# Performance work log

Hardware: AMD Instinct MI355X
Metric: run time of the kernel (lower is better)

Reference implementation:

```python
import jax, jax.numpy as jnp
import numpy as np

NEG_SLOPE = 0.2
BN_EPS = 1e-5


def gat_conv(x, src, dst, num_nodes, W, att_src, att_dst, bias, concat):
    # x: [N, F_in]; W: [F_in, H*C]; att_src/att_dst: [H, C]
    H, C = att_src.shape
    h = (x @ W).reshape(num_nodes, H, C)                 # [N, H, C]
    a_src = jnp.einsum('nhc,hc->nh', h, att_src)          # [N, H]
    a_dst = jnp.einsum('nhc,hc->nh', h, att_dst)          # [N, H]
    e = a_src[src] + a_dst[dst]                           # [E, H]
    e = jax.nn.leaky_relu(e, NEG_SLOPE)
    # segment softmax over edges sharing the same destination node
    m = jax.ops.segment_max(e, dst, num_segments=num_nodes)   # [N, H]
    ex = jnp.exp(e - m[dst])
    denom = jax.ops.segment_sum(ex, dst, num_segments=num_nodes)  # [N, H]
    alpha = ex / (denom[dst] + 1e-16)                     # [E, H]
    msg = h[src] * alpha[:, :, None]                      # [E, H, C]
    out = jax.ops.segment_sum(msg, dst, num_segments=num_nodes)   # [N, H, C]
    if concat:
        return out.reshape(num_nodes, H * C) + bias
    return out.mean(axis=1) + bias


def batch_norm(x, gamma, beta):
    mu = x.mean(axis=0)
    var = x.var(axis=0)
    return (x - mu) * jax.lax.rsqrt(var + BN_EPS) * gamma + beta


def setup_inputs() -> dict:
    key = jax.random.key(0)
    ks = jax.random.split(key, 16)
    N, E, F_in, C, H, NC = 50000, 800000, 128, 16, 8, 2
    s = lambda k, shape, fan: jax.random.normal(k, shape, jnp.float32) * (1.0 / np.sqrt(fan))
    inp = {
        'x': jax.random.normal(ks[0], (N, F_in), jnp.float32),
        'edge_index': jax.random.randint(ks[1], (2, E), 0, N, jnp.int32),
        'W0': s(ks[2], (F_in, H * C), F_in),
        'att_src0': s(ks[3], (H, C), C),
        'att_dst0': s(ks[4], (H, C), C),
        'b0': jnp.zeros((H * C,), jnp.float32),
        'gamma0': jnp.ones((H * C,), jnp.float32),
        'beta0': jnp.zeros((H * C,), jnp.float32),
        'W1': s(ks[5], (H * C, H * C), H * C),
        'att_src1': s(ks[6], (H, C), C),
        'att_dst1': s(ks[7], (H, C), C),
        'b1': jnp.zeros((C,), jnp.float32),
        'gamma1': jnp.ones((C,), jnp.float32),
        'beta1': jnp.zeros((C,), jnp.float32),
        'Wc': s(ks[8], (C, NC), C),
        'bc': jnp.zeros((NC,), jnp.float32),
    }
    return inp


def reference(x, edge_index, W0, att_src0, att_dst0, b0, gamma0, beta0,
              W1, att_src1, att_dst1, b1, gamma1, beta1, Wc, bc):
    N = x.shape[0]
    loop = jnp.arange(N, dtype=edge_index.dtype)
    src = jnp.concatenate([edge_index[0], loop])  # add self-loops (PyG default)
    dst = jnp.concatenate([edge_index[1], loop])
    # layer 0: concat heads -> [N, H*C]
    h = gat_conv(x, src, dst, N, W0, att_src0, att_dst0, b0, concat=True)
    h = batch_norm(h, gamma0, beta0)
    h = jax.nn.elu(h)
    # layer 1: average heads -> [N, C]
    h = gat_conv(h, src, dst, N, W1, att_src1, att_dst1, b1, concat=False)
    h = batch_norm(h, gamma1, beta1)
    logits = h @ Wc + bc
    return logits
```

## Files before the change

kernel.cpp:

```cpp
#include <hip/hip_runtime.h>
#include <math.h>

#define NEG_SLOPE 0.2f
#define BN_EPS 1e-5f


__device__ __forceinline__ void edge_sd(const int* __restrict__ ei, int E, int eid, int& s, int& d) {
    if (eid < E) { s = ei[eid]; d = ei[E + eid]; }
    else         { s = d = eid - E; }
}

__device__ __forceinline__ float lrelu(float v) { return v > 0.f ? v : NEG_SLOPE * v; }

__device__ __forceinline__ unsigned short f2bf(float f) {
    unsigned u = __float_as_uint(f);
    u += 0x7fffu + ((u >> 16) & 1u);
    return (unsigned short)(u >> 16);
}

__global__ __launch_bounds__(256) void gemm128(const float* __restrict__ X,
                                               const float* __restrict__ W,
                                               unsigned short* __restrict__ Ybf,
                                               const float* __restrict__ att_s,
                                               const float* __restrict__ att_d,
                                               float* __restrict__ a_srcO,
                                               float* __restrict__ a_dstO,
                                               const float* __restrict__ bnmu,
                                               const float* __restrict__ bnrs,
                                               const float* __restrict__ gamma,
                                               const float* __restrict__ beta,
                                               int Nrows) {
    __shared__ float xs[64 * 128];
    int bm = blockIdx.x * 64;
    int tid = threadIdx.x;

    const float4* Xv = (const float4*)(X + (size_t)bm * 128);
    float4* xsv = (float4*)xs;
    if (bnmu == nullptr) {
        for (int i = tid; i < 64 * 32; i += 256) {
            int row = i >> 5;
            xsv[i] = (bm + row < Nrows) ? Xv[i] : make_float4(0.f, 0.f, 0.f, 0.f);
        }
    } else {
        for (int i = tid; i < 64 * 32; i += 256) {
            int row = i >> 5;
            int cb = (i & 31) * 4;
            float4 v = (bm + row < Nrows) ? Xv[i] : make_float4(0.f, 0.f, 0.f, 0.f);
            float4 m4 = *(const float4*)(bnmu + cb);
            float4 r4 = *(const float4*)(bnrs + cb);
            float4 g4 = *(const float4*)(gamma + cb);
            float4 b4 = *(const float4*)(beta + cb);
            v.x = (v.x - m4.x) * r4.x * g4.x + b4.x;
            v.y = (v.y - m4.y) * r4.y * g4.y + b4.y;
            v.z = (v.z - m4.z) * r4.z * g4.z + b4.z;
            v.w = (v.w - m4.w) * r4.w * g4.w + b4.w;
            v.x = v.x > 0.f ? v.x : expm1f(v.x);
            v.y = v.y > 0.f ? v.y : expm1f(v.y);
            v.z = v.z > 0.f ? v.z : expm1f(v.z);
            v.w = v.w > 0.f ? v.w : expm1f(v.w);
            xsv[i] = v;
        }
    }
    __syncthreads();

    int cq = tid & 31;
    int rg = tid >> 5;
    int lane = tid & 63;

    float acc[8][4];
#pragma unroll
    for (int r = 0; r < 8; r++)
#pragma unroll
        for (int j = 0; j < 4; j++) acc[r][j] = 0.f;

    const float* xbase = xs + (rg * 8) * 128;
#pragma unroll 2
    for (int k4 = 0; k4 < 32; k4++) {
        const float* wrow = W + k4 * 4 * 128 + cq * 4;
        float4 w0 = *(const float4*)(wrow);
        float4 w1 = *(const float4*)(wrow + 128);
        float4 w2 = *(const float4*)(wrow + 256);
        float4 w3 = *(const float4*)(wrow + 384);
#pragma unroll
        for (int r = 0; r < 8; r++) {
            float4 x4 = *(const float4*)(xbase + r * 128 + k4 * 4);
            acc[r][0] += x4.x * w0.x; acc[r][1] += x4.x * w0.y;
            acc[r][2] += x4.x * w0.z; acc[r][3] += x4.x * w0.w;
            acc[r][0] += x4.y * w1.x; acc[r][1] += x4.y * w1.y;
            acc[r][2] += x4.y * w1.z; acc[r][3] += x4.y * w1.w;
            acc[r][0] += x4.z * w2.x; acc[r][1] += x4.z * w2.y;
            acc[r][2] += x4.z * w2.z; acc[r][3] += x4.z * w2.w;
            acc[r][0] += x4.w * w3.x; acc[r][1] += x4.w * w3.y;
            acc[r][2] += x4.w * w3.z; acc[r][3] += x4.w * w3.w;
        }
    }

    int h = cq >> 2;
    float4 as4 = *(const float4*)(att_s + h * 16 + (cq & 3) * 4);
    float4 ad4 = *(const float4*)(att_d + h * 16 + (cq & 3) * 4);

#pragma unroll
    for (int r = 0; r < 8; r++) {
        int row = bm + rg * 8 + r;
        float ps = acc[r][0] * as4.x + acc[r][1] * as4.y + acc[r][2] * as4.z + acc[r][3] * as4.w;
        float pd = acc[r][0] * ad4.x + acc[r][1] * ad4.y + acc[r][2] * ad4.z + acc[r][3] * ad4.w;
        ps += __shfl_xor(ps, 1); ps += __shfl_xor(ps, 2);
        pd += __shfl_xor(pd, 1); pd += __shfl_xor(pd, 2);
        if (row < Nrows) {
            ushort4 pk;
            pk.x = f2bf(acc[r][0]);
            pk.y = f2bf(acc[r][1]);
            pk.z = f2bf(acc[r][2]);
            pk.w = f2bf(acc[r][3]);
            *(ushort4*)(Ybf + (size_t)row * 128 + cq * 4) = pk;
            if ((lane & 3) == 0) {
                a_srcO[row * 8 + h] = ps;
                a_dstO[row * 8 + h] = pd;
            }
        }
    }
}

__global__ void hist_kernel(const int* __restrict__ ei, int E, int Etot,
                            int* __restrict__ counts, int* __restrict__ rank) {
    int eid = blockIdx.x * 256 + threadIdx.x;
    if (eid >= Etot) return;
    int s, d;
    edge_sd(ei, E, eid, s, d);
    rank[eid] = atomicAdd(&counts[d], 1);
}

__global__ __launch_bounds__(256) void chunksum_kernel(const int* __restrict__ counts,
                                                       int* __restrict__ csum, int N) {
    __shared__ int red[256];
    int base = blockIdx.x * 1024;
    int s = 0;
    for (int i = threadIdx.x; i < 1024; i += 256) {
        int idx = base + i;
        s += (idx < N) ? counts[idx] : 0;
    }
    red[threadIdx.x] = s;
    __syncthreads();
#pragma unroll
    for (int st = 128; st > 0; st >>= 1) {
        if (threadIdx.x < st) red[threadIdx.x] += red[threadIdx.x + st];
        __syncthreads();
    }
    if (threadIdx.x == 0) csum[blockIdx.x] = red[0];
}

__global__ void chunkscan_kernel(int* __restrict__ csum, int nchunk) {
    int lane = threadIdx.x;
    int v = (lane < nchunk) ? csum[lane] : 0;
    int incl = v;
#pragma unroll
    for (int off = 1; off < 64; off <<= 1) {
        int t = __shfl_up(incl, off);
        if (lane >= off) incl += t;
    }
    if (lane < nchunk) csum[lane] = incl - v;
}

__global__ __launch_bounds__(1024) void scanfinal_kernel(const int* __restrict__ counts,
                                                         const int* __restrict__ csum,
                                                         int* __restrict__ rowptr, int N) {
    __shared__ int wsum[16], woff_s[16];
    int tid = threadIdx.x, lane = tid & 63, wid = tid >> 6;
    int idx = blockIdx.x * 1024 + tid;
    int v = (idx < N) ? counts[idx] : 0;
    int incl = v;
#pragma unroll
    for (int off = 1; off < 64; off <<= 1) {
        int t = __shfl_up(incl, off);
        if (lane >= off) incl += t;
    }
    if (lane == 63) wsum[wid] = incl;
    __syncthreads();
    if (wid == 0 && lane < 16) {
        int w = wsum[lane], iw = w;
#pragma unroll
        for (int off = 1; off < 16; off <<= 1) {
            int t = __shfl_up(iw, off);
            if (lane >= off) iw += t;
        }
        woff_s[lane] = iw - w;
    }
    __syncthreads();
    if (idx < N) rowptr[idx + 1] = csum[blockIdx.x] + woff_s[wid] + incl;
    if (blockIdx.x == 0 && tid == 0) rowptr[0] = 0;
}

__global__ void scatter_kernel(const int* __restrict__ ei, int E, int Etot,
                               const int* __restrict__ rowptr, const int* __restrict__ rank,
                               unsigned short* __restrict__ ssrc) {
    int eid = blockIdx.x * 256 + threadIdx.x;
    if (eid >= Etot) return;
    int s, d;
    edge_sd(ei, E, eid, s, d);
    ssrc[rowptr[d] + rank[eid]] = (unsigned short)s;
}

template <bool MEAN>
__global__ __launch_bounds__(256) void agg_kernel(const int* __restrict__ rowptr,
                                                  const unsigned short* __restrict__ ssrc,
                                                  const float* __restrict__ a_src,
                                                  const float* __restrict__ a_dst,
                                                  const unsigned short* __restrict__ Hbf,
                                                  float* __restrict__ outbuf, int N) {
    int wid = threadIdx.x >> 6;
    int dst = blockIdx.x * 4 + wid;
    if (dst >= N) return;
    int lane = threadIdx.x & 63;
    int j  = lane >> 3;
    int hj = lane & 7;
    int hf = lane >> 3;
    int f  = lane * 2;
    int start = rowptr[dst], end = rowptr[dst + 1];
    float adst = a_dst[dst * 8 + hj];

    float acc0 = 0.f, acc1 = 0.f, denl = 0.f;

    int i = start + j;
    int s = (i < end) ? (int)ssrc[i] : -1;
    float ar = (s >= 0) ? a_src[s * 8 + hj] : 0.f;

    for (int base = start; base < end; base += 8) {
        int sA[8];
#pragma unroll
        for (int j2 = 0; j2 < 8; j2++) sA[j2] = __shfl(s, j2 * 8);
        unsigned uA[8];
#pragma unroll
        for (int j2 = 0; j2 < 8; j2++)
            uA[j2] = (sA[j2] >= 0) ? *(const unsigned*)(Hbf + (size_t)sA[j2] * 128 + f) : 0u;

        int inext = base + 8 + j;
        int snext = (inext < end) ? (int)ssrc[inext] : -1;
        float anext = (snext >= 0) ? a_src[snext * 8 + hj] : 0.f;

        float w = (s >= 0) ? __expf(lrelu(ar + adst)) : 0.f;
        denl += w;
        float wA[8];
#pragma unroll
        for (int j2 = 0; j2 < 8; j2++) wA[j2] = __shfl(w, j2 * 8 + hf);

#pragma unroll
        for (int j2 = 0; j2 < 8; j2++) {
            acc0 += wA[j2] * __uint_as_float(uA[j2] << 16);
            acc1 += wA[j2] * __uint_as_float(uA[j2] & 0xffff0000u);
        }
        s = snext;
        ar = anext;
    }
#pragma unroll
    for (int off = 8; off < 64; off <<= 1) denl += __shfl_xor(denl, off);
    float den = __shfl(denl, hf);
    float inv = 1.f / (den + 1e-16f);
    if (!MEAN) {
        *(float2*)(outbuf + (size_t)dst * 128 + f) = make_float2(acc0 * inv, acc1 * inv);
    } else {
        float r0 = acc0 * inv, r1 = acc1 * inv;
#pragma unroll
        for (int off = 8; off < 64; off <<= 1) {
            r0 += __shfl_xor(r0, off);
            r1 += __shfl_xor(r1, off);
        }
        if (lane < 8)
            *(float2*)(outbuf + (size_t)dst * 16 + lane * 2) =
                make_float2(r0 * 0.125f, r1 * 0.125f);
    }
}

template <int C>
__global__ __launch_bounds__(256) void stats_part_kernel(const float* __restrict__ X, int Nrows,
                                                         float* __restrict__ partial,
                                                         int rows_per_block) {
    constexpr int GSZ = 256 / C;
    __shared__ float ls[256], lq[256];
    int c = threadIdx.x % C;
    int g = threadIdx.x / C;
    long base = (long)blockIdx.x * rows_per_block;
    long endr = base + rows_per_block;
    if (endr > Nrows) endr = Nrows;
    float s = 0.f, q = 0.f;
    for (long r = base + g; r < endr; r += GSZ) {
        float v = X[r * C + c];
        s += v;
        q += v * v;
    }
    ls[threadIdx.x] = s;
    lq[threadIdx.x] = q;
    __syncthreads();
#pragma unroll
    for (int st = GSZ / 2; st > 0; st >>= 1) {
        if (g < st) {
            ls[threadIdx.x] += ls[threadIdx.x + st * C];
            lq[threadIdx.x] += lq[threadIdx.x + st * C];
        }
        __syncthreads();
    }
    if (g == 0) {
        partial[(size_t)blockIdx.x * (2 * C) + c] = ls[c];
        partial[(size_t)blockIdx.x * (2 * C) + C + c] = lq[c];
    }
}

template <int C>
__global__ __launch_bounds__(1024) void stats_final_kernel(const float* __restrict__ partial,
                                                           int nblk, float invN,
                                                           float* __restrict__ mu,
                                                           float* __restrict__ rsig) {
    constexpr int G = 1024 / C;
    __shared__ float ls[1024], lq[1024];
    int c = threadIdx.x % C;
    int g = threadIdx.x / C;
    float s = 0.f, q = 0.f;
    for (int b = g; b < nblk; b += G) {
        s += partial[(size_t)b * (2 * C) + c];
        q += partial[(size_t)b * (2 * C) + C + c];
    }
    ls[threadIdx.x] = s;
    lq[threadIdx.x] = q;
    __syncthreads();
#pragma unroll
    for (int st = G / 2; st > 0; st >>= 1) {
        if (g < st) {
            ls[threadIdx.x] += ls[threadIdx.x + st * C];
            lq[threadIdx.x] += lq[threadIdx.x + st * C];
        }
        __syncthreads();
    }
    if (g == 0) {
        float m_ = ls[c] * invN;
        float v = lq[c] * invN - m_ * m_;
        mu[c] = m_;
        rsig[c] = rsqrtf(v + BN_EPS);
    }
}

__global__ void final_kernel(const float* __restrict__ out1,
                             const float* __restrict__ mu, const float* __restrict__ rsig,
                             const float* __restrict__ gamma, const float* __restrict__ beta,
                             const float* __restrict__ Wc, const float* __restrict__ bc,
                             float* __restrict__ out, int N) {
    int n = blockIdx.x * 256 + threadIdx.x;
    if (n >= N) return;
    float l0 = bc[0], l1 = bc[1];
#pragma unroll
    for (int c = 0; c < 16; c++) {
        float v = (out1[(size_t)n * 16 + c] - mu[c]) * rsig[c] * gamma[c] + beta[c];
        l0 += v * Wc[c * 2 + 0];
        l1 += v * Wc[c * 2 + 1];
    }
    out[(size_t)n * 2 + 0] = l0;
    out[(size_t)n * 2 + 1] = l1;
}

extern "C" void kernel_launch(void* const* d_in, const int* in_sizes, int n_in,
                              void* d_out, int out_size, void* d_ws, size_t ws_size,
                              hipStream_t stream) {
    const float* x   = (const float*)d_in[0];
    const int*   ei  = (const int*)d_in[1];
    const float* W0  = (const float*)d_in[2];
    const float* as0 = (const float*)d_in[3];
    const float* ad0 = (const float*)d_in[4];
    const float* g0  = (const float*)d_in[6];
    const float* be0 = (const float*)d_in[7];
    const float* W1  = (const float*)d_in[8];
    const float* as1 = (const float*)d_in[9];
    const float* ad1 = (const float*)d_in[10];
    const float* g1  = (const float*)d_in[12];
    const float* be1 = (const float*)d_in[13];
    const float* Wc  = (const float*)d_in[14];
    const float* bc  = (const float*)d_in[15];
    float* out = (float*)d_out;

    int N = in_sizes[0] / 128;
    int E = in_sizes[1] / 2;
    int Etot = E + N;

    char* ws = (char*)d_ws;
    size_t off = 0;
    auto walloc = [&](size_t bytes) -> void* {
        void* p = ws + off;
        off += (bytes + 255) & ~(size_t)255;
        return p;
    };
    float*          B       = (float*)walloc((size_t)N * 128 * 4);
    unsigned short* Hbf     = (unsigned short*)walloc((size_t)N * 128 * 2);
    float*          a_src   = (float*)walloc((size_t)N * 8 * 4);
    float*          a_dst   = (float*)walloc((size_t)N * 8 * 4);
    float*          out1    = (float*)walloc((size_t)N * 16 * 4);
    int*            counts  = (int*)walloc((size_t)N * 4);
    int*            rowptr  = (int*)walloc((size_t)(N + 1) * 4);
    int*            rank    = (int*)walloc((size_t)Etot * 4);
    int*            csum    = (int*)walloc(64 * 4);
    unsigned short* ssrc    = (unsigned short*)walloc((size_t)Etot * 2);
    float*          partial = (float*)walloc((size_t)256 * 256 * 4);
    float*          stats   = (float*)walloc(2 * 128 * 4);
    float* mu = stats, * rsig = stats + 128;

    dim3 b256(256);
    int gN64    = (N + 63) / 64;
    int gE      = (Etot + 255) / 256;
    int gAgg    = (N + 3) / 4;
    int nchunk  = (N + 1023) / 1024;
    const int SBLK = 256;
    int rpb = (N + SBLK - 1) / SBLK;

    hipMemsetAsync(counts, 0, (size_t)N * 4, stream);
    hist_kernel<<<gE, b256, 0, stream>>>(ei, E, Etot, counts, rank);
    chunksum_kernel<<<nchunk, b256, 0, stream>>>(counts, csum, N);
    chunkscan_kernel<<<1, 64, 0, stream>>>(csum, nchunk);
    scanfinal_kernel<<<nchunk, 1024, 0, stream>>>(counts, csum, rowptr, N);
    scatter_kernel<<<gE, b256, 0, stream>>>(ei, E, Etot, rowptr, rank, ssrc);

    gemm128<<<gN64, b256, 0, stream>>>(x, W0, Hbf, as0, ad0, a_src, a_dst,
                                       nullptr, nullptr, nullptr, nullptr, N);
    agg_kernel<false><<<gAgg, b256, 0, stream>>>(rowptr, ssrc, a_src, a_dst, Hbf, B, N);
    stats_part_kernel<128><<<SBLK, b256, 0, stream>>>(B, N, partial, rpb);
    stats_final_kernel<128><<<1, 1024, 0, stream>>>(partial, SBLK, 1.0f / N, mu, rsig);

    gemm128<<<gN64, b256, 0, stream>>>(B, W1, Hbf, as1, ad1, a_src, a_dst,
                                       mu, rsig, g0, be0, N);
    agg_kernel<true><<<gAgg, b256, 0, stream>>>(rowptr, ssrc, a_src, a_dst, Hbf, out1, N);
    stats_part_kernel<16><<<SBLK, b256, 0, stream>>>(out1, N, partial, rpb);
    stats_final_kernel<16><<<1, 1024, 0, stream>>>(partial, SBLK, 1.0f / N, mu, rsig);
    final_kernel<<<(N + 255) / 256, b256, 0, stream>>>(out1, mu, rsig, g1, be1, Wc, bc, out, N);
}
```

Baseline: 346.8 us.

## Restructure node GEMM with column-split grid, transposed weights, swizzled LDS tile

The 128-wide GEMM is split across 4 column groups via blockIdx.y. Each thread now computes one row by 8 columns, reading pre-transposed weights (a new small transpose kernel runs each call) as wave-uniform float4 loads. X tiles in LDS use an XOR swizzle to avoid bank conflicts on per-row reads. Attention dot products are reduced through LDS and the bf16 outputs are staged for coalesced 16-byte stores. The catch is that each block reloads and re-normalizes the full 64x128 X tile 4 times, and a kernel launch is added.

After: 496.0 us. +43.0%, slower.

```diff
diff --git a/kernel.cpp b/kernel.cpp
--- a/kernel.cpp
+++ b/kernel.cpp
@@ -18,8 +18,22 @@
     return (unsigned short)(u >> 16);
 }
 
+__global__ __launch_bounds__(256) void transpose_kernel(const float* __restrict__ W0,
+                                                        const float* __restrict__ W1,
+                                                        float* __restrict__ T0,
+                                                        float* __restrict__ T1) {
+    int b = blockIdx.x;
+    const float* S = (b & 4) ? W1 : W0;
+    float*       T = (b & 4) ? T1 : T0;
+    int part = b & 3;
+    for (int i = threadIdx.x; i < 4096; i += 256) {
+        int idx = part * 4096 + i;
+        T[(idx & 127) * 128 + (idx >> 7)] = S[idx];
+    }
+}
+
 __global__ __launch_bounds__(256) void gemm128(const float* __restrict__ X,
-                                               const float* __restrict__ W,
+                                               const float* __restrict__ Wt,
                                                unsigned short* __restrict__ Ybf,
                                                const float* __restrict__ att_s,
                                                const float* __restrict__ att_d,
@@ -32,19 +46,21 @@
                                                int Nrows) {
     __shared__ float xs[64 * 128];
     int bm = blockIdx.x * 64;
+    int cg = blockIdx.y;
     int tid = threadIdx.x;
 
     const float4* Xv = (const float4*)(X + (size_t)bm * 128);
     float4* xsv = (float4*)xs;
     if (bnmu == nullptr) {
-        for (int i = tid; i < 64 * 32; i += 256) {
-            int row = i >> 5;
-            xsv[i] = (bm + row < Nrows) ? Xv[i] : make_float4(0.f, 0.f, 0.f, 0.f);
+        for (int i = tid; i < 2048; i += 256) {
+            int row = i >> 5, c = i & 31;
+            float4 v = (bm + row < Nrows) ? Xv[i] : make_float4(0.f, 0.f, 0.f, 0.f);
+            xsv[((row << 5) | c) ^ (row & 7)] = v;
         }
     } else {
-        for (int i = tid; i < 64 * 32; i += 256) {
-            int row = i >> 5;
-            int cb = (i & 31) * 4;
+        for (int i = tid; i < 2048; i += 256) {
+            int row = i >> 5, c = i & 31;
+            int cb = c * 4;
             float4 v = (bm + row < Nrows) ? Xv[i] : make_float4(0.f, 0.f, 0.f, 0.f);
             float4 m4 = *(const float4*)(bnmu + cb);
             float4 r4 = *(const float4*)(bnrs + cb);
@@ -58,65 +74,74 @@
             v.y = v.y > 0.f ? v.y : expm1f(v.y);
             v.z = v.z > 0.f ? v.z : expm1f(v.z);
             v.w = v.w > 0.f ? v.w : expm1f(v.w);
-            xsv[i] = v;
-        }
-    }
-    __syncthreads();
-
-    int cq = tid & 31;
-    int rg = tid >> 5;
+            xsv[((row << 5) | c) ^ (row & 7)] = v;
+        }
+    }
+    __syncthreads();
+
+    int w = tid >> 6;
     int lane = tid & 63;
-
-    float acc[8][4];
-#pragma unroll
-    for (int r = 0; r < 8; r++)
-#pragma unroll
-        for (int j = 0; j < 4; j++) acc[r][j] = 0.f;
-
-    const float* xbase = xs + (rg * 8) * 128;
+    int c0 = cg * 32 + w * 8;
+
+    float acc[8];
+#pragma unroll
+    for (int j = 0; j < 8; j++) acc[j] = 0.f;
+
+    const float4* xr = (const float4*)xs;
+    const float* wbase = Wt + (size_t)c0 * 128;
+
 #pragma unroll 2
     for (int k4 = 0; k4 < 32; k4++) {
-        const float* wrow = W + k4 * 4 * 128 + cq * 4;
-        float4 w0 = *(const float4*)(wrow);
-        float4 w1 = *(const float4*)(wrow + 128);
-        float4 w2 = *(const float4*)(wrow + 256);
-        float4 w3 = *(const float4*)(wrow + 384);
-#pragma unroll
-        for (int r = 0; r < 8; r++) {
-            float4 x4 = *(const float4*)(xbase + r * 128 + k4 * 4);
-            acc[r][0] += x4.x * w0.x; acc[r][1] += x4.x * w0.y;
-            acc[r][2] += x4.x * w0.z; acc[r][3] += x4.x * w0.w;
-            acc[r][0] += x4.y * w1.x; acc[r][1] += x4.y * w1.y;
-            acc[r][2] += x4.y * w1.z; acc[r][3] += x4.y * w1.w;
-            acc[r][0] += x4.z * w2.x; acc[r][1] += x4.z * w2.y;
-            acc[r][2] += x4.z * w2.z; acc[r][3] += x4.z * w2.w;
-            acc[r][0] += x4.w * w3.x; acc[r][1] += x4.w * w3.y;
-            acc[r][2] += x4.w * w3.z; acc[r][3] += x4.w * w3.w;
-        }
-    }
-
-    int h = cq >> 2;
-    float4 as4 = *(const float4*)(att_s + h * 16 + (cq & 3) * 4);
-    float4 ad4 = *(const float4*)(att_d + h * 16 + (cq & 3) * 4);
-
-#pragma unroll
-    for (int r = 0; r < 8; r++) {
-        int row = bm + rg * 8 + r;
-        float ps = acc[r][0] * as4.x + acc[r][1] * as4.y + acc[r][2] * as4.z + acc[r][3] * as4.w;
-        float pd = acc[r][0] * ad4.x + acc[r][1] * ad4.y + acc[r][2] * ad4.z + acc[r][3] * ad4.w;
-        ps += __shfl_xor(ps, 1); ps += __shfl_xor(ps, 2);
-        pd += __shfl_xor(pd, 1); pd += __shfl_xor(pd, 2);
-        if (row < Nrows) {
-            ushort4 pk;
-            pk.x = f2bf(acc[r][0]);
-            pk.y = f2bf(acc[r][1]);
-            pk.z = f2bf(acc[r][2]);
-            pk.w = f2bf(acc[r][3]);
-            *(ushort4*)(Ybf + (size_t)row * 128 + cq * 4) = pk;
-            if ((lane & 3) == 0) {
-                a_srcO[row * 8 + h] = ps;
-                a_dstO[row * 8 + h] = pd;
-            }
+        float4 x4 = xr[((lane << 5) | k4) ^ (lane & 7)];
+#pragma unroll
+        for (int j = 0; j < 8; j++) {
+            float4 wj = *(const float4*)(wbase + j * 128 + k4 * 4);
+            acc[j] += x4.x * wj.x;
+            acc[j] += x4.y * wj.y;
+            acc[j] += x4.z * wj.z;
+            acc[j] += x4.w * wj.w;
+        }
+    }
+
+    __syncthreads();
+    float* sred = xs;
+    unsigned short* outls = (unsigned short*)(xs + 512);
+
+    int h = cg * 2 + (w >> 1);
+    int ao = (w & 1) * 8;
+    float4 asl = *(const float4*)(att_s + h * 16 + ao);
+    float4 ash = *(const float4*)(att_s + h * 16 + ao + 4);
+    float4 adl = *(const float4*)(att_d + h * 16 + ao);
+    float4 adh = *(const float4*)(att_d + h * 16 + ao + 4);
+    float ps = acc[0] * asl.x + acc[1] * asl.y + acc[2] * asl.z + acc[3] * asl.w
+             + acc[4] * ash.x + acc[5] * ash.y + acc[6] * ash.z + acc[7] * ash.w;
+    float pd = acc[0] * adl.x + acc[1] * adl.y + acc[2] * adl.z + acc[3] * adl.w
+             + acc[4] * adh.x + acc[5] * adh.y + acc[6] * adh.z + acc[7] * adh.w;
+    sred[(w * 64 + lane) * 2]     = ps;
+    sred[(w * 64 + lane) * 2 + 1] = pd;
+
+    ushort4 p0, p1;
+    p0.x = f2bf(acc[0]); p0.y = f2bf(acc[1]); p0.z = f2bf(acc[2]); p0.w = f2bf(acc[3]);
+    p1.x = f2bf(acc[4]); p1.y = f2bf(acc[5]); p1.z = f2bf(acc[6]); p1.w = f2bf(acc[7]);
+    *(ushort4*)(outls + lane * 32 + w * 8)     = p0;
+    *(ushort4*)(outls + lane * 32 + w * 8 + 4) = p1;
+    __syncthreads();
+
+    if (tid < 128) {
+        int r = tid & 63, p = tid >> 6;
+        if (bm + r < Nrows) {
+            float s0 = sred[((2 * p) * 64 + r) * 2]     + sred[((2 * p + 1) * 64 + r) * 2];
+            float d0 = sred[((2 * p) * 64 + r) * 2 + 1] + sred[((2 * p + 1) * 64 + r) * 2 + 1];
+            int hh = cg * 2 + p;
+            a_srcO[(size_t)(bm + r) * 8 + hh] = s0;
+            a_dstO[(size_t)(bm + r) * 8 + hh] = d0;
+        }
+    }
+    {
+        int r = tid >> 2, ch = tid & 3;
+        if (bm + r < Nrows) {
+            uint4 v = *(uint4*)(outls + r * 32 + ch * 8);
+            *(uint4*)(Ybf + (size_t)(bm + r) * 128 + cg * 32 + ch * 8) = v;
         }
     }
 }
@@ -397,15 +422,20 @@
     unsigned short* ssrc    = (unsigned short*)walloc((size_t)Etot * 2);
     float*          partial = (float*)walloc((size_t)256 * 256 * 4);
     float*          stats   = (float*)walloc(2 * 128 * 4);
+    float*          Wt0     = (float*)walloc((size_t)128 * 128 * 4);
+    float*          Wt1     = (float*)walloc((size_t)128 * 128 * 4);
     float* mu = stats, * rsig = stats + 128;
 
     dim3 b256(256);
     int gN64    = (N + 63) / 64;
+    dim3 gGemm(gN64, 4);
     int gE      = (Etot + 255) / 256;
     int gAgg    = (N + 3) / 4;
     int nchunk  = (N + 1023) / 1024;
     const int SBLK = 256;
     int rpb = (N + SBLK - 1) / SBLK;
+
+    transpose_kernel<<<8, b256, 0, stream>>>(W0, W1, Wt0, Wt1);
 
     hipMemsetAsync(counts, 0, (size_t)N * 4, stream);
     hist_kernel<<<gE, b256, 0, stream>>>(ei, E, Etot, counts, rank);
@@ -414,14 +444,14 @@
     scanfinal_kernel<<<nchunk, 1024, 0, stream>>>(counts, csum, rowptr, N);
     scatter_kernel<<<gE, b256, 0, stream>>>(ei, E, Etot, rowptr, rank, ssrc);
 
-    gemm128<<<gN64, b256, 0, stream>>>(x, W0, Hbf, as0, ad0, a_src, a_dst,
-                                       nullptr, nullptr, nullptr, nullptr, N);
+    gemm128<<<gGemm, b256, 0, stream>>>(x, Wt0, Hbf, as0, ad0, a_src, a_dst,
+                                        nullptr, nullptr, nullptr, nullptr, N);
     agg_kernel<false><<<gAgg, b256, 0, stream>>>(rowptr, ssrc, a_src, a_dst, Hbf, B, N);
     stats_part_kernel<128><<<SBLK, b256, 0, stream>>>(B, N, partial, rpb);
     stats_final_kernel<128><<<1, 1024, 0, stream>>>(partial, SBLK, 1.0f / N, mu, rsig);
 
-    gemm128<<<gN64, b256, 0, stream>>>(B, W1, Hbf, as1, ad1, a_src, a_dst,
-                                       mu, rsig, g0, be0, N);
+    gemm128<<<gGemm, b256, 0, stream>>>(B, Wt1, Hbf, as1, ad1, a_src, a_dst,
+                                        mu, rsig, g0, be0, N);
     agg_kernel<true><<<gAgg, b256, 0, stream>>>(rowptr, ssrc, a_src, a_dst, Hbf, out1, N);
     stats_part_kernel<16><<<SBLK, b256, 0, stream>>>(out1, N, partial, rpb);
     stats_final_kernel<16><<<1, 1024, 0, stream>>>(partial, SBLK, 1.0f / N, mu, rsig);
```

## Use split-bf16 MFMA (3-term) for the dense GEMMs instead of FP32 FMA

Applied to the files above, without the earlier changes.

The two 128x128 node-feature GEMMs now run on matrix cores with bf16 MFMA instructions. Activations and weights are split into high and low bf16 parts, and three MFMAs per tile keep accuracy close to fp32. A small pre-kernel splits and transposes W0 and W1 into hi/lo bf16 buffers. Results are staged in LDS to compute the attention projections and the bf16 output. The aim is to remove the FP32 FMA-bound GEMM cost, at the price of extra conversion work and a slight loss of precision.

Result: slower. 369.1 us (+6.4%).

```diff
diff --git a/kernel.cpp b/kernel.cpp
--- a/kernel.cpp
+++ b/kernel.cpp
@@ -3,6 +3,9 @@
 
 #define NEG_SLOPE 0.2f
 #define BN_EPS 1e-5f
+
+typedef __attribute__((ext_vector_type(8))) short short8v;
+typedef __attribute__((ext_vector_type(4))) float f32x4;
 
 
 __device__ __forceinline__ void edge_sd(const int* __restrict__ ei, int E, int eid, int& s, int& d) {
@@ -17,9 +20,35 @@
     u += 0x7fffu + ((u >> 16) & 1u);
     return (unsigned short)(u >> 16);
 }
+__device__ __forceinline__ float bfval(unsigned short u) {
+    return __uint_as_float(((unsigned)u) << 16);
+}
+
+__global__ __launch_bounds__(256) void wsplit_kernel(const float* __restrict__ W0,
+                                                     const float* __restrict__ W1,
+                                                     unsigned short* __restrict__ H0,
+                                                     unsigned short* __restrict__ L0,
+                                                     unsigned short* __restrict__ H1,
+                                                     unsigned short* __restrict__ L1) {
+    int b = blockIdx.x;
+    const float* S = (b & 4) ? W1 : W0;
+    unsigned short* H = (b & 4) ? H1 : H0;
+    unsigned short* L = (b & 4) ? L1 : L0;
+    int part = b & 3;
+    for (int i = threadIdx.x; i < 4096; i += 256) {
+        int idx = part * 4096 + i;
+        int k = idx >> 7, c = idx & 127;
+        float v = S[idx];
+        unsigned short h = f2bf(v);
+        unsigned short l = f2bf(v - bfval(h));
+        H[c * 128 + k] = h;
+        L[c * 128 + k] = l;
+    }
+}
 
 __global__ __launch_bounds__(256) void gemm128(const float* __restrict__ X,
-                                               const float* __restrict__ W,
+                                               const unsigned short* __restrict__ Wthi,
+                                               const unsigned short* __restrict__ Wtlo,
                                                unsigned short* __restrict__ Ybf,
                                                const float* __restrict__ att_s,
                                                const float* __restrict__ att_d,
@@ -30,92 +59,108 @@
                                                const float* __restrict__ gamma,
                                                const float* __restrict__ beta,
                                                int Nrows) {
-    __shared__ float xs[64 * 128];
+    __shared__ float hs[64 * 128];
     int bm = blockIdx.x * 64;
     int tid = threadIdx.x;
-
-    const float4* Xv = (const float4*)(X + (size_t)bm * 128);
-    float4* xsv = (float4*)xs;
-    if (bnmu == nullptr) {
-        for (int i = tid; i < 64 * 32; i += 256) {
-            int row = i >> 5;
-            xsv[i] = (bm + row < Nrows) ? Xv[i] : make_float4(0.f, 0.f, 0.f, 0.f);
-        }
-    } else {
-        for (int i = tid; i < 64 * 32; i += 256) {
-            int row = i >> 5;
-            int cb = (i & 31) * 4;
-            float4 v = (bm + row < Nrows) ? Xv[i] : make_float4(0.f, 0.f, 0.f, 0.f);
-            float4 m4 = *(const float4*)(bnmu + cb);
-            float4 r4 = *(const float4*)(bnrs + cb);
-            float4 g4 = *(const float4*)(gamma + cb);
-            float4 b4 = *(const float4*)(beta + cb);
-            v.x = (v.x - m4.x) * r4.x * g4.x + b4.x;
-            v.y = (v.y - m4.y) * r4.y * g4.y + b4.y;
-            v.z = (v.z - m4.z) * r4.z * g4.z + b4.z;
-            v.w = (v.w - m4.w) * r4.w * g4.w + b4.w;
-            v.x = v.x > 0.f ? v.x : expm1f(v.x);
-            v.y = v.y > 0.f ? v.y : expm1f(v.y);
-            v.z = v.z > 0.f ? v.z : expm1f(v.z);
-            v.w = v.w > 0.f ? v.w : expm1f(v.w);
-            xsv[i] = v;
-        }
-    }
-    __syncthreads();
-
-    int cq = tid & 31;
-    int rg = tid >> 5;
-    int lane = tid & 63;
-
-    float acc[8][4];
-#pragma unroll
-    for (int r = 0; r < 8; r++)
-#pragma unroll
-        for (int j = 0; j < 4; j++) acc[r][j] = 0.f;
-
-    const float* xbase = xs + (rg * 8) * 128;
-#pragma unroll 2
-    for (int k4 = 0; k4 < 32; k4++) {
-        const float* wrow = W + k4 * 4 * 128 + cq * 4;
-        float4 w0 = *(const float4*)(wrow);
-        float4 w1 = *(const float4*)(wrow + 128);
-        float4 w2 = *(const float4*)(wrow + 256);
-        float4 w3 = *(const float4*)(wrow + 384);
-#pragma unroll
-        for (int r = 0; r < 8; r++) {
-            float4 x4 = *(const float4*)(xbase + r * 128 + k4 * 4);
-            acc[r][0] += x4.x * w0.x; acc[r][1] += x4.x * w0.y;
-            acc[r][2] += x4.x * w0.z; acc[r][3] += x4.x * w0.w;
-            acc[r][0] += x4.y * w1.x; acc[r][1] += x4.y * w1.y;
-            acc[r][2] += x4.y * w1.z; acc[r][3] += x4.y * w1.w;
-            acc[r][0] += x4.z * w2.x; acc[r][1] += x4.z * w2.y;
-            acc[r][2] += x4.z * w2.z; acc[r][3] += x4.z * w2.w;
-            acc[r][0] += x4.w * w3.x; acc[r][1] += x4.w * w3.y;
-            acc[r][2] += x4.w * w3.z; acc[r][3] += x4.w * w3.w;
-        }
-    }
-
-    int h = cq >> 2;
-    float4 as4 = *(const float4*)(att_s + h * 16 + (cq & 3) * 4);
-    float4 ad4 = *(const float4*)(att_d + h * 16 + (cq & 3) * 4);
-
-#pragma unroll
-    for (int r = 0; r < 8; r++) {
-        int row = bm + rg * 8 + r;
-        float ps = acc[r][0] * as4.x + acc[r][1] * as4.y + acc[r][2] * as4.z + acc[r][3] * as4.w;
-        float pd = acc[r][0] * ad4.x + acc[r][1] * ad4.y + acc[r][2] * ad4.z + acc[r][3] * ad4.w;
-        ps += __shfl_xor(ps, 1); ps += __shfl_xor(ps, 2);
-        pd += __shfl_xor(pd, 1); pd += __shfl_xor(pd, 2);
-        if (row < Nrows) {
-            ushort4 pk;
-            pk.x = f2bf(acc[r][0]);
-            pk.y = f2bf(acc[r][1]);
-            pk.z = f2bf(acc[r][2]);
-            pk.w = f2bf(acc[r][3]);
-            *(ushort4*)(Ybf + (size_t)row * 128 + cq * 4) = pk;
-            if ((lane & 3) == 0) {
-                a_srcO[row * 8 + h] = ps;
-                a_dstO[row * 8 + h] = pd;
+    int w = tid >> 6, lane = tid & 63;
+    int li = lane & 15, g = lane >> 4;
+    int row = bm + w * 16 + li;
+    bool rok = row < Nrows;
+    const float* xp = X + (size_t)row * 128;
+
+    f32x4 acc[8];
+#pragma unroll
+    for (int ct = 0; ct < 8; ct++) acc[ct] = (f32x4){0.f, 0.f, 0.f, 0.f};
+
+#pragma unroll
+    for (int kc = 0; kc < 4; kc++) {
+        int kb = kc * 32 + g * 8;
+        float xv[8];
+        if (rok) {
+            float4 x0 = *(const float4*)(xp + kb);
+            float4 x1 = *(const float4*)(xp + kb + 4);
+            xv[0] = x0.x; xv[1] = x0.y; xv[2] = x0.z; xv[3] = x0.w;
+            xv[4] = x1.x; xv[5] = x1.y; xv[6] = x1.z; xv[7] = x1.w;
+        } else {
+#pragma unroll
+            for (int e = 0; e < 8; e++) xv[e] = 0.f;
+        }
+        if (bnmu != nullptr) {
+            float mv[8], rv[8], gv[8], bv[8];
+            *(float4*)(mv)     = *(const float4*)(bnmu + kb);
+            *(float4*)(mv + 4) = *(const float4*)(bnmu + kb + 4);
+            *(float4*)(rv)     = *(const float4*)(bnrs + kb);
+            *(float4*)(rv + 4) = *(const float4*)(bnrs + kb + 4);
+            *(float4*)(gv)     = *(const float4*)(gamma + kb);
+            *(float4*)(gv + 4) = *(const float4*)(gamma + kb + 4);
+            *(float4*)(bv)     = *(const float4*)(beta + kb);
+            *(float4*)(bv + 4) = *(const float4*)(beta + kb + 4);
+#pragma unroll
+            for (int e = 0; e < 8; e++) {
+                float t = (xv[e] - mv[e]) * rv[e] * gv[e] + bv[e];
+                xv[e] = t > 0.f ? t : expm1f(t);
+            }
+        }
+        short8v ah, al;
+#pragma unroll
+        for (int e = 0; e < 8; e++) {
+            unsigned short hb = f2bf(xv[e]);
+            ah[e] = (short)hb;
+            al[e] = (short)f2bf(xv[e] - bfval(hb));
+        }
+        const unsigned short* wb  = Wthi + (size_t)li * 128 + kb;
+        const unsigned short* wlb = Wtlo + (size_t)li * 128 + kb;
+#pragma unroll
+        for (int ct = 0; ct < 8; ct++) {
+            short8v bh = *(const short8v*)(wb  + ct * 2048);
+            short8v bl = *(const short8v*)(wlb + ct * 2048);
+            acc[ct] = __builtin_amdgcn_mfma_f32_16x16x32_bf16(ah, bh, acc[ct], 0, 0, 0);
+            acc[ct] = __builtin_amdgcn_mfma_f32_16x16x32_bf16(ah, bl, acc[ct], 0, 0, 0);
+            acc[ct] = __builtin_amdgcn_mfma_f32_16x16x32_bf16(al, bh, acc[ct], 0, 0, 0);
+        }
+    }
+
+#pragma unroll
+    for (int ct = 0; ct < 8; ct++)
+#pragma unroll
+        for (int r = 0; r < 4; r++)
+            hs[(w * 16 + g * 4 + r) * 128 + ct * 16 + li] = acc[ct][r];
+    __syncthreads();
+
+#pragma unroll
+    for (int p0 = 0; p0 < 2; p0++) {
+        int p = tid + p0 * 256;
+        int r = p >> 3, hh = p & 7;
+        if (bm + r < Nrows) {
+            const float4* hp4 = (const float4*)(hs + r * 128 + hh * 16);
+            const float4* as4 = (const float4*)(att_s + hh * 16);
+            const float4* ad4 = (const float4*)(att_d + hh * 16);
+            float ss = 0.f, sd = 0.f;
+#pragma unroll
+            for (int q = 0; q < 4; q++) {
+                float4 v = hp4[q], s4 = as4[q], d4 = ad4[q];
+                ss += v.x * s4.x + v.y * s4.y + v.z * s4.z + v.w * s4.w;
+                sd += v.x * d4.x + v.y * d4.y + v.z * d4.z + v.w * d4.w;
+            }
+            a_srcO[(size_t)(bm + r) * 8 + hh] = ss;
+            a_dstO[(size_t)(bm + r) * 8 + hh] = sd;
+        }
+    }
+
+    {
+        int r = tid >> 2, seg = tid & 3;
+        if (bm + r < Nrows) {
+            const float* hp = hs + r * 128 + seg * 32;
+#pragma unroll
+            for (int q = 0; q < 4; q++) {
+                float4 a = *(const float4*)(hp + q * 8);
+                float4 b = *(const float4*)(hp + q * 8 + 4);
+                uint4 o;
+                o.x = (unsigned)f2bf(a.x) | ((unsigned)f2bf(a.y) << 16);
+                o.y = (unsigned)f2bf(a.z) | ((unsigned)f2bf(a.w) << 16);
+                o.z = (unsigned)f2bf(b.x) | ((unsigned)f2bf(b.y) << 16);
+                o.w = (unsigned)f2bf(b.z) | ((unsigned)f2bf(b.w) << 16);
+                *(uint4*)(Ybf + (size_t)(bm + r) * 128 + seg * 32 + q * 8) = o;
             }
         }
     }
@@ -397,6 +442,10 @@
     unsigned short* ssrc    = (unsigned short*)walloc((size_t)Etot * 2);
     float*          partial = (float*)walloc((size_t)256 * 256 * 4);
     float*          stats   = (float*)walloc(2 * 128 * 4);
+    unsigned short* Whi0    = (unsigned short*)walloc((size_t)128 * 128 * 2);
+    unsigned short* Wlo0    = (unsigned short*)walloc((size_t)128 * 128 * 2);
+    unsigned short* Whi1    = (unsigned short*)walloc((size_t)128 * 128 * 2);
+    unsigned short* Wlo1    = (unsigned short*)walloc((size_t)128 * 128 * 2);
     float* mu = stats, * rsig = stats + 128;
 
     dim3 b256(256);
@@ -407,6 +456,8 @@
     const int SBLK = 256;
     int rpb = (N + SBLK - 1) / SBLK;
 
+    wsplit_kernel<<<8, b256, 0, stream>>>(W0, W1, Whi0, Wlo0, Whi1, Wlo1);
+
     hipMemsetAsync(counts, 0, (size_t)N * 4, stream);
     hist_kernel<<<gE, b256, 0, stream>>>(ei, E, Etot, counts, rank);
     chunksum_kernel<<<nchunk, b256, 0, stream>>>(counts, csum, N);
@@ -414,13 +465,13 @@
     scanfinal_kernel<<<nchunk, 1024, 0, stream>>>(counts, csum, rowptr, N);
     scatter_kernel<<<gE, b256, 0, stream>>>(ei, E, Etot, rowptr, rank, ssrc);
 
-    gemm128<<<gN64, b256, 0, stream>>>(x, W0, Hbf, as0, ad0, a_src, a_dst,
+    gemm128<<<gN64, b256, 0, stream>>>(x, Whi0, Wlo0, Hbf, as0, ad0, a_src, a_dst,
                                        nullptr, nullptr, nullptr, nullptr, N);
     agg_kernel<false><<<gAgg, b256, 0, stream>>>(rowptr, ssrc, a_src, a_dst, Hbf, B, N);
     stats_part_kernel<128><<<SBLK, b256, 0, stream>>>(B, N, partial, rpb);
     stats_final_kernel<128><<<1, 1024, 0, stream>>>(partial, SBLK, 1.0f / N, mu, rsig);
 
-    gemm128<<<gN64, b256, 0, stream>>>(B, W1, Hbf, as1, ad1, a_src, a_dst,
+    gemm128<<<gN64, b256, 0, stream>>>(B, Whi1, Wlo1, Hbf, as1, ad1, a_src, a_dst,
                                        mu, rsig, g0, be0, N);
     agg_kernel<true><<<gAgg, b256, 0, stream>>>(rowptr, ssrc, a_src, a_dst, Hbf, out1, N);
     stats_part_kernel<16><<<SBLK, b256, 0, stream>>>(out1, N, partial, rpb);
```
